# Kernel optimization log

Hardware: AMD Instinct MI355X
Metric: run time of the kernel (lower is better)

Reference implementation:

```python
import jax, jax.numpy as jnp
import numpy as np

NEG_SLOPE = 0.2

def gat_conv(x, src, dst, W, att_src, att_dst, bias, heads, out_c, concat):
    # x: [N, F_in]; src/dst: [E] (self-loops already included)
    N = x.shape[0]
    xh = (x @ W).reshape(N, heads, out_c)               # [N,H,C]
    a_src = jnp.sum(xh * att_src, axis=-1)              # [N,H]
    a_dst = jnp.sum(xh * att_dst, axis=-1)              # [N,H]
    alpha = a_src[src] + a_dst[dst]                     # [E,H]
    alpha = jax.nn.leaky_relu(alpha, NEG_SLOPE)
    # segment softmax over destination node
    m = jax.ops.segment_max(alpha, dst, num_segments=N) # [N,H]
    e = jnp.exp(alpha - m[dst])                         # [E,H]
    s = jax.ops.segment_sum(e, dst, num_segments=N)     # [N,H]
    coef = e / s[dst]                                   # [E,H]
    msg = xh[src] * coef[:, :, None]                    # [E,H,C]
    out = jax.ops.segment_sum(msg, dst, num_segments=N) # [N,H,C]
    if concat:
        out = out.reshape(N, heads * out_c)
    else:
        out = out.mean(axis=1)
    return out + bias

def setup_inputs() -> dict:
    key = jax.random.key(0)
    ks = jax.random.split(key, 12)
    N, E = 50000, 400000
    Fin, Hc, H, Fout = 128, 16, 8, 128
    x = jax.random.normal(ks[0], (N, Fin), dtype=jnp.float32)
    src = jax.random.randint(ks[1], (E,), 0, N, dtype=jnp.int32)
    dst = jax.random.randint(ks[2], (E,), 0, N, dtype=jnp.int32)
    g = lambda k, shp, fan: (jax.random.normal(k, shp, dtype=jnp.float32) * (1.0 / np.sqrt(fan))).astype(jnp.float32)
    return {
        'x': x, 'src': src, 'dst': dst,
        'W1': g(ks[3], (Fin, H * Hc), Fin),
        'att_src1': g(ks[4], (H, Hc), Hc),
        'att_dst1': g(ks[5], (H, Hc), Hc),
        'b1': jnp.zeros((H * Hc,), dtype=jnp.float32),
        'W2': g(ks[6], (H * Hc, Fout), H * Hc),
        'att_src2': g(ks[7], (1, Fout), Fout),
        'att_dst2': g(ks[8], (1, Fout), Fout),
        'b2': jnp.zeros((Fout,), dtype=jnp.float32),
    }

def reference(x, src, dst, W1, att_src1, att_dst1, b1, W2, att_src2, att_dst2, b2):
    N = x.shape[0]
    loops = jnp.arange(N, dtype=src.dtype)
    s = jnp.concatenate([src, loops])  # add_self_loops=True (PyG default)
    d = jnp.concatenate([dst, loops])
    h = gat_conv(x, s, d, W1, att_src1, att_dst1, b1, heads=8, out_c=16, concat=True)
    h = jax.nn.elu(h)
    out = gat_conv(h, s, d, W2, att_src2, att_dst2, b2, heads=1, out_c=128, concat=False)
    return out
```

## Files before the change

kernel.cpp:

```cpp
#include <hip/hip_runtime.h>
#include <hip/hip_bf16.h>
#include <math.h>

#define NEG_SLOPE 0.2f
#define SCAN_BLOCK 256
#define BK 32
#define LOG2E 1.4426950408889634f

__device__ __forceinline__ unsigned pack_bf16_pair(float lo, float hi) {
    unsigned ul = __float_as_uint(lo);
    ul += 0x7fffu + ((ul >> 16) & 1u);
    unsigned uh = __float_as_uint(hi);
    uh += 0x7fffu + ((uh >> 16) & 1u);
    return (ul >> 16) | (uh & 0xffff0000u);
}

__global__ __launch_bounds__(256) void zero_int_kernel(int* __restrict__ p, int n) {
    int i = blockIdx.x * 256 + threadIdx.x;
    if (i < n) p[i] = 0;
}

__global__ __launch_bounds__(256) void count_deg_kernel(const int* __restrict__ dst,
                                                        int E, int N, int* __restrict__ deg) {
    int e = blockIdx.x * 256 + threadIdx.x;
    int Etot = E + N;
    if (e >= Etot) return;
    int d = (e < E) ? dst[e] : (e - E);
    atomicAdd(&deg[d], 1);
}

__global__ __launch_bounds__(SCAN_BLOCK) void deg_partial_kernel(const int* __restrict__ deg,
                                                                 int* __restrict__ part, int N) {
    __shared__ int red[SCAN_BLOCK];
    int t = threadIdx.x;
    int i = blockIdx.x * SCAN_BLOCK + t;
    red[t] = (i < N) ? deg[i] : 0;
    __syncthreads();
    #pragma unroll
    for (int off = SCAN_BLOCK / 2; off > 0; off >>= 1) {
        if (t < off) red[t] += red[t + off];
        __syncthreads();
    }
    if (t == 0) part[blockIdx.x] = red[0];
}

__global__ __launch_bounds__(1024) void scan_part_kernel(int* __restrict__ part, int nPart) {
    __shared__ int s[1024];
    int t = threadIdx.x;
    int v = (t < nPart) ? part[t] : 0;
    s[t] = v;
    __syncthreads();
    for (int off = 1; off < 1024; off <<= 1) {
        int u = (t >= off) ? s[t - off] : 0;
        __syncthreads();
        s[t] += u;
        __syncthreads();
    }
    if (t < nPart) part[t] = (t == 0) ? 0 : s[t - 1];
}

__global__ __launch_bounds__(SCAN_BLOCK) void scan_final_kernel(const int* __restrict__ deg,
                                                                const int* __restrict__ part,
                                                                int* __restrict__ row_ptr, int N) {
    __shared__ int s[SCAN_BLOCK];
    int t = threadIdx.x;
    int i = blockIdx.x * SCAN_BLOCK + t;
    int v = (i < N) ? deg[i] : 0;
    s[t] = v;
    __syncthreads();
    #pragma unroll
    for (int off = 1; off < SCAN_BLOCK; off <<= 1) {
        int u = (t >= off) ? s[t - off] : 0;
        __syncthreads();
        s[t] += u;
        __syncthreads();
    }
    int incl = s[t];
    int base = part[blockIdx.x];
    if (i < N) row_ptr[i] = base + incl - v;
    if (i == N - 1) row_ptr[N] = base + incl;
}

__global__ __launch_bounds__(256) void scatter_kernel(const int* __restrict__ src,
                                                      const int* __restrict__ dst,
                                                      int E, int N,
                                                      const int* __restrict__ row_ptr,
                                                      int* __restrict__ cursor,
                                                      int* __restrict__ col_src) {
    int e = blockIdx.x * 256 + threadIdx.x;
    int Etot = E + N;
    if (e >= Etot) return;
    int d, s;
    if (e < E) { d = dst[e]; s = src[e]; } else { d = e - E; s = e - E; }
    int pos = atomicAdd(&cursor[d], 1);
    col_src[row_ptr[d] + pos] = s;
}

__global__ __launch_bounds__(128) void gemm_rb_kernel(const float* __restrict__ X,
                                                      const float* __restrict__ W,
                                                      float* __restrict__ Y,
                                                      unsigned* __restrict__ Ybf, int N) {
    __shared__ float Xs[BK][68];
    __shared__ float Wt[BK][128];
    const int t = threadIdx.x;
    const int r0 = blockIdx.x * 64;
    const int lane = t & 63, w = t >> 6;
    const int lx = lane & 15, ly = lane >> 4;
    const int row_base = w * 32 + ly * 8;
    const int c1 = lx * 4, c2 = 64 + lx * 4;

    float acc[8][8];
    #pragma unroll
    for (int i = 0; i < 8; ++i)
        #pragma unroll
        for (int j = 0; j < 8; ++j) acc[i][j] = 0.f;

    for (int kt = 0; kt < 128; kt += BK) {
        __syncthreads();
        #pragma unroll
        for (int i = 0; i < 4; ++i) {
            int idx = i * 128 + t;
            int row = idx >> 3, k4 = idx & 7;
            int gr = r0 + row;
            float4 g = make_float4(0.f, 0.f, 0.f, 0.f);
            if (gr < N) g = *(const float4*)(X + (size_t)gr * 128 + kt + k4 * 4);
            Xs[k4 * 4 + 0][row] = g.x;
            Xs[k4 * 4 + 1][row] = g.y;
            Xs[k4 * 4 + 2][row] = g.z;
            Xs[k4 * 4 + 3][row] = g.w;
        }
        #pragma unroll
        for (int i = 0; i < 8; ++i) {
            int idx = i * 128 + t;
            int wr = idx >> 5, c4 = idx & 31;
            *(float4*)&Wt[wr][c4 * 4] = *(const float4*)(W + (size_t)(kt + wr) * 128 + c4 * 4);
        }
        __syncthreads();

        #pragma unroll 8
        for (int k = 0; k < BK; ++k) {
            float4 a0 = *(const float4*)&Xs[k][row_base];
            float4 a1 = *(const float4*)&Xs[k][row_base + 4];
            float4 b0 = *(const float4*)&Wt[k][c1];
            float4 b1 = *(const float4*)&Wt[k][c2];
            float a[8] = {a0.x, a0.y, a0.z, a0.w, a1.x, a1.y, a1.z, a1.w};
            float b[8] = {b0.x, b0.y, b0.z, b0.w, b1.x, b1.y, b1.z, b1.w};
            #pragma unroll
            for (int i = 0; i < 8; ++i)
                #pragma unroll
                for (int j = 0; j < 8; ++j)
                    acc[i][j] = fmaf(a[i], b[j], acc[i][j]);
        }
    }

    #pragma unroll
    for (int i = 0; i < 8; ++i) {
        int gr = r0 + row_base + i;
        if (gr < N) {
            *(float4*)(Y + (size_t)gr * 128 + c1) =
                make_float4(acc[i][0], acc[i][1], acc[i][2], acc[i][3]);
            *(float4*)(Y + (size_t)gr * 128 + c2) =
                make_float4(acc[i][4], acc[i][5], acc[i][6], acc[i][7]);
            uint4 pk;
            pk.x = pack_bf16_pair(acc[i][0], acc[i][4]);
            pk.y = pack_bf16_pair(acc[i][1], acc[i][5]);
            pk.z = pack_bf16_pair(acc[i][2], acc[i][6]);
            pk.w = pack_bf16_pair(acc[i][3], acc[i][7]);
            *(uint4*)(Ybf + (size_t)gr * 64 + c1) = pk;
        }
    }
}

__global__ __launch_bounds__(256) void attdot1_kernel(const float* __restrict__ xh,
                                                      const float* __restrict__ attS,
                                                      const float* __restrict__ attD,
                                                      float* __restrict__ asrc,
                                                      float* __restrict__ adst, int N) {
    int node = blockIdx.x * 4 + (threadIdx.x >> 6);
    int lane = threadIdx.x & 63;
    if (node >= N) return;
    const float* row = xh + (size_t)node * 128;
    float x1 = row[lane], x2 = row[lane + 64];
    float s1 = x1 * attS[lane], s2 = x2 * attS[lane + 64];
    float d1 = x1 * attD[lane], d2 = x2 * attD[lane + 64];
    #pragma unroll
    for (int off = 8; off >= 1; off >>= 1) {
        s1 += __shfl_xor(s1, off, 64);
        s2 += __shfl_xor(s2, off, 64);
        d1 += __shfl_xor(d1, off, 64);
        d2 += __shfl_xor(d2, off, 64);
    }
    if ((lane & 15) == 0) {
        int h = lane >> 4;
        asrc[node * 8 + h]     = s1;
        asrc[node * 8 + h + 4] = s2;
        adst[node * 8 + h]     = d1;
        adst[node * 8 + h + 4] = d2;
    }
}

__global__ __launch_bounds__(256) void attdot2_kernel(const float* __restrict__ xh,
                                                      const float* __restrict__ attS,
                                                      const float* __restrict__ attD,
                                                      float* __restrict__ asrc,
                                                      float* __restrict__ adst, int N) {
    int node = blockIdx.x * 4 + (threadIdx.x >> 6);
    int lane = threadIdx.x & 63;
    if (node >= N) return;
    const float* row = xh + (size_t)node * 128;
    float x1 = row[lane], x2 = row[lane + 64];
    float ts = x1 * attS[lane] + x2 * attS[lane + 64];
    float td = x1 * attD[lane] + x2 * attD[lane + 64];
    #pragma unroll
    for (int off = 32; off >= 1; off >>= 1) {
        ts += __shfl_xor(ts, off, 64);
        td += __shfl_xor(td, off, 64);
    }
    if (lane == 0) { asrc[node] = ts; adst[node] = td; }
}

__global__ __launch_bounds__(256) void agg1_kernel(const unsigned* __restrict__ xhp,
                                                   const float* __restrict__ asrc,
                                                   const float* __restrict__ adst,
                                                   const int* __restrict__ row_ptr,
                                                   const int* __restrict__ col_src,
                                                   const float* __restrict__ b1,
                                                   float* __restrict__ out, int N) {
    int node = blockIdx.x * 4 + (threadIdx.x >> 6);
    int lane = threadIdx.x & 63;
    if (node >= N) return;
    const int grp = lane >> 4;
    const int lx = lane & 15;
    const int gbase = lane & 48;
    float ad1 = adst[node * 8 + grp];
    float ad2 = adst[node * 8 + grp + 4];
    int beg = row_ptr[node], end = row_ptr[node + 1];
    int deg = end - beg;

    float s1 = 0.f, s2 = 0.f, acc1 = 0.f, acc2 = 0.f;

    if (deg <= 16) {
        bool valid = lx < deg;
        int sv = col_src[valid ? (beg + lx) : beg];
        float al1 = asrc[sv * 8 + grp] + ad1;
        float al2 = asrc[sv * 8 + grp + 4] + ad2;
        al1 = fmaxf(al1, NEG_SLOPE * al1);
        al2 = fmaxf(al2, NEG_SLOPE * al2);
        float m1 = valid ? al1 : -1e30f;
        float m2 = valid ? al2 : -1e30f;
        #pragma unroll
        for (int off = 1; off < 16; off <<= 1) {
            m1 = fmaxf(m1, __shfl_xor(m1, off, 64));
            m2 = fmaxf(m2, __shfl_xor(m2, off, 64));
        }
        float p1 = valid ? exp2f((al1 - m1) * LOG2E) : 0.f;
        float p2 = valid ? exp2f((al2 - m2) * LOG2E) : 0.f;
        #pragma unroll 4
        for (int i = 0; i < deg; ++i) {
            int   svi = __shfl(sv, gbase + i, 64);
            float q1  = __shfl(p1, gbase + i, 64);
            float q2  = __shfl(p2, gbase + i, 64);
            unsigned v = xhp[(size_t)svi * 64 + lane];
            float x1 = __uint_as_float(v << 16);
            float x2 = __uint_as_float(v & 0xffff0000u);
            s1 += q1; acc1 = fmaf(q1, x1, acc1);
            s2 += q2; acc2 = fmaf(q2, x2, acc2);
        }
    } else {
        float m1 = -1e30f, m2 = -1e30f;
        for (int c = beg; c < end; c += 16) {
            int e = c + lx;
            bool valid = e < end;
            int sv = col_src[valid ? e : beg];
            float al1 = asrc[sv * 8 + grp] + ad1;
            float al2 = asrc[sv * 8 + grp + 4] + ad2;
            al1 = fmaxf(al1, NEG_SLOPE * al1);
            al2 = fmaxf(al2, NEG_SLOPE * al2);
            if (valid) { m1 = fmaxf(m1, al1); m2 = fmaxf(m2, al2); }
        }
        #pragma unroll
        for (int off = 1; off < 16; off <<= 1) {
            m1 = fmaxf(m1, __shfl_xor(m1, off, 64));
            m2 = fmaxf(m2, __shfl_xor(m2, off, 64));
        }
        for (int c = beg; c < end; c += 16) {
            int e = c + lx;
            bool valid = e < end;
            int sv = col_src[valid ? e : beg];
            float al1 = asrc[sv * 8 + grp] + ad1;
            float al2 = asrc[sv * 8 + grp + 4] + ad2;
            al1 = fmaxf(al1, NEG_SLOPE * al1);
            al2 = fmaxf(al2, NEG_SLOPE * al2);
            float p1 = valid ? exp2f((al1 - m1) * LOG2E) : 0.f;
            float p2 = valid ? exp2f((al2 - m2) * LOG2E) : 0.f;
            int cnt = min(16, end - c);
            #pragma unroll 4
            for (int i = 0; i < cnt; ++i) {
                int   svi = __shfl(sv, gbase + i, 64);
                float q1  = __shfl(p1, gbase + i, 64);
                float q2  = __shfl(p2, gbase + i, 64);
                unsigned v = xhp[(size_t)svi * 64 + lane];
                float x1 = __uint_as_float(v << 16);
                float x2 = __uint_as_float(v & 0xffff0000u);
                s1 += q1; acc1 = fmaf(q1, x1, acc1);
                s2 += q2; acc2 = fmaf(q2, x2, acc2);
            }
        }
    }

    float o1 = acc1 / s1 + b1[lane];
    float o2 = acc2 / s2 + b1[lane + 64];
    o1 = (o1 > 0.f) ? o1 : (__expf(o1) - 1.f);
    o2 = (o2 > 0.f) ? o2 : (__expf(o2) - 1.f);
    out[(size_t)node * 128 + lane]      = o1;
    out[(size_t)node * 128 + lane + 64] = o2;
}

__global__ __launch_bounds__(256) void agg2_kernel(const unsigned* __restrict__ xhp,
                                                   const float* __restrict__ asrc,
                                                   const float* __restrict__ adst,
                                                   const int* __restrict__ row_ptr,
                                                   const int* __restrict__ col_src,
                                                   const float* __restrict__ b2,
                                                   float* __restrict__ out, int N) {
    int node = blockIdx.x * 4 + (threadIdx.x >> 6);
    int lane = threadIdx.x & 63;
    if (node >= N) return;
    float ad = adst[node];
    int beg = row_ptr[node], end = row_ptr[node + 1];
    int deg = end - beg;

    float s = 0.f, acc1 = 0.f, acc2 = 0.f;

    if (deg <= 64) {
        bool valid = lane < deg;
        int sv = col_src[valid ? (beg + lane) : beg];
        float al = asrc[sv] + ad;
        al = fmaxf(al, NEG_SLOPE * al);
        float m = valid ? al : -1e30f;
        #pragma unroll
        for (int off = 1; off < 64; off <<= 1)
            m = fmaxf(m, __shfl_xor(m, off, 64));
        float p = valid ? exp2f((al - m) * LOG2E) : 0.f;
        #pragma unroll 4
        for (int i = 0; i < deg; ++i) {
            int   svi = __shfl(sv, i, 64);
            float q   = __shfl(p, i, 64);
            unsigned v = xhp[(size_t)svi * 64 + lane];
            float x1 = __uint_as_float(v << 16);
            float x2 = __uint_as_float(v & 0xffff0000u);
            s += q;
            acc1 = fmaf(q, x1, acc1);
            acc2 = fmaf(q, x2, acc2);
        }
    } else {
        float m = -1e30f;
        for (int c = beg; c < end; c += 64) {
            int e = c + lane;
            bool valid = e < end;
            int sv = col_src[valid ? e : beg];
            float al = asrc[sv] + ad;
            al = fmaxf(al, NEG_SLOPE * al);
            if (valid) m = fmaxf(m, al);
        }
        #pragma unroll
        for (int off = 1; off < 64; off <<= 1)
            m = fmaxf(m, __shfl_xor(m, off, 64));
        for (int c = beg; c < end; c += 64) {
            int e = c + lane;
            bool valid = e < end;
            int sv = col_src[valid ? e : beg];
            float al = asrc[sv] + ad;
            al = fmaxf(al, NEG_SLOPE * al);
            float p = valid ? exp2f((al - m) * LOG2E) : 0.f;
            int cnt = min(64, end - c);
            #pragma unroll 4
            for (int i = 0; i < cnt; ++i) {
                int   svi = __shfl(sv, i, 64);
                float q   = __shfl(p, i, 64);
                unsigned v = xhp[(size_t)svi * 64 + lane];
                float x1 = __uint_as_float(v << 16);
                float x2 = __uint_as_float(v & 0xffff0000u);
                s += q;
                acc1 = fmaf(q, x1, acc1);
                acc2 = fmaf(q, x2, acc2);
            }
        }
    }

    out[(size_t)node * 128 + lane]      = acc1 / s + b2[lane];
    out[(size_t)node * 128 + lane + 64] = acc2 / s + b2[lane + 64];
}

extern "C" void kernel_launch(void* const* d_in, const int* in_sizes, int n_in,
                              void* d_out, int out_size, void* d_ws, size_t ws_size,
                              hipStream_t stream) {
    const float* x        = (const float*)d_in[0];
    const int*   src      = (const int*)d_in[1];
    const int*   dst      = (const int*)d_in[2];
    const float* W1       = (const float*)d_in[3];
    const float* att_src1 = (const float*)d_in[4];
    const float* att_dst1 = (const float*)d_in[5];
    const float* b1       = (const float*)d_in[6];
    const float* W2       = (const float*)d_in[7];
    const float* att_src2 = (const float*)d_in[8];
    const float* att_dst2 = (const float*)d_in[9];
    const float* b2       = (const float*)d_in[10];

    const int N = in_sizes[0] / 128;
    const int E = in_sizes[1];
    const int Etot = E + N;

    float* fws   = (float*)d_ws;
    float* xh    = fws;
    float* asrc1 = xh + (size_t)N * 128;
    float* adst1 = asrc1 + (size_t)N * 8;
    float* asrc2 = adst1 + (size_t)N * 8;
    float* adst2 = asrc2 + N;
    int*   deg     = (int*)(adst2 + N);
    int*   cursor  = deg + N;
    int*   row_ptr = cursor + N;
    int*   col_src = row_ptr + N + 1;
    int*   part    = col_src + Etot;
    unsigned* xhp  = (unsigned*)(part + 1024);

    float* h = (float*)d_out;

    const int nodeBlocks = (N + 3) / 4;
    const int edgeBlocks = (Etot + 255) / 256;
    const int gemmBlocks = (N + 63) / 64;
    const int scanBlocks = (N + SCAN_BLOCK - 1) / SCAN_BLOCK;

    zero_int_kernel<<<(2 * N + 255) / 256, 256, 0, stream>>>(deg, 2 * N);
    count_deg_kernel<<<edgeBlocks, 256, 0, stream>>>(dst, E, N, deg);
    deg_partial_kernel<<<scanBlocks, SCAN_BLOCK, 0, stream>>>(deg, part, N);
    scan_part_kernel<<<1, 1024, 0, stream>>>(part, scanBlocks);
    scan_final_kernel<<<scanBlocks, SCAN_BLOCK, 0, stream>>>(deg, part, row_ptr, N);
    scatter_kernel<<<edgeBlocks, 256, 0, stream>>>(src, dst, E, N, row_ptr, cursor, col_src);

    gemm_rb_kernel<<<gemmBlocks, 128, 0, stream>>>(x, W1, xh, xhp, N);
    attdot1_kernel<<<nodeBlocks, 256, 0, stream>>>(xh, att_src1, att_dst1, asrc1, adst1, N);
    agg1_kernel<<<nodeBlocks, 256, 0, stream>>>(xhp, asrc1, adst1, row_ptr, col_src, b1, h, N);

    gemm_rb_kernel<<<gemmBlocks, 128, 0, stream>>>(h, W2, xh, xhp, N);
    attdot2_kernel<<<nodeBlocks, 256, 0, stream>>>(xh, att_src2, att_dst2, asrc2, adst2, N);
    agg2_kernel<<<nodeBlocks, 256, 0, stream>>>(xhp, asrc2, adst2, row_ptr, col_src, b2, (float*)d_out, N);
}
```

Baseline: 311.9 us.

## Fuse attention dot products into GEMM epilogue and drop fp32 xh output

The attention-coefficient dot products (a_src, a_dst) are now computed in the GEMM epilogue from register accumulators using shuffles, replacing the separate attdot kernels. The fp32 xh output is no longer written, so only the bf16 copy used by aggregation is stored. The GEMM block also goes to 256 threads with 4x8 tiles per thread to raise occupancy. This removes two launches and a full N x 128 fp32 write and re-read per layer, at the cost of shuffle work in the epilogue and a smaller per-thread tile.

```diff
diff --git a/kernel.cpp b/kernel.cpp
--- a/kernel.cpp
+++ b/kernel.cpp
@@ -96,30 +96,37 @@
     col_src[row_ptr[d] + pos] = s;
 }
 
-__global__ __launch_bounds__(128) void gemm_rb_kernel(const float* __restrict__ X,
-                                                      const float* __restrict__ W,
-                                                      float* __restrict__ Y,
-                                                      unsigned* __restrict__ Ybf, int N) {
+__global__ __launch_bounds__(256) void gemm_fused_kernel(const float* __restrict__ X,
+                                                         const float* __restrict__ W,
+                                                         const float* __restrict__ attS,
+                                                         const float* __restrict__ attD,
+                                                         unsigned* __restrict__ Ybf,
+                                                         float* __restrict__ asrc,
+                                                         float* __restrict__ adst,
+                                                         int N, int heads) {
     __shared__ float Xs[BK][68];
     __shared__ float Wt[BK][128];
+    __shared__ float attSs[128], attDs[128];
     const int t = threadIdx.x;
     const int r0 = blockIdx.x * 64;
-    const int lane = t & 63, w = t >> 6;
+    const int lane = t & 63, wv = t >> 6;
     const int lx = lane & 15, ly = lane >> 4;
-    const int row_base = w * 32 + ly * 8;
+    const int row_base = wv * 16 + ly * 4;
     const int c1 = lx * 4, c2 = 64 + lx * 4;
 
-    float acc[8][8];
+    if (t < 128) { attSs[t] = attS[t]; attDs[t] = attD[t]; }
+
+    float acc[4][8];
     #pragma unroll
-    for (int i = 0; i < 8; ++i)
+    for (int i = 0; i < 4; ++i)
         #pragma unroll
         for (int j = 0; j < 8; ++j) acc[i][j] = 0.f;
 
     for (int kt = 0; kt < 128; kt += BK) {
         __syncthreads();
         #pragma unroll
-        for (int i = 0; i < 4; ++i) {
-            int idx = i * 128 + t;
+        for (int i = 0; i < 2; ++i) {
+            int idx = i * 256 + t;
             int row = idx >> 3, k4 = idx & 7;
             int gr = r0 + row;
             float4 g = make_float4(0.f, 0.f, 0.f, 0.f);
@@ -130,8 +137,8 @@
             Xs[k4 * 4 + 3][row] = g.w;
         }
         #pragma unroll
-        for (int i = 0; i < 8; ++i) {
-            int idx = i * 128 + t;
+        for (int i = 0; i < 4; ++i) {
+            int idx = i * 256 + t;
             int wr = idx >> 5, c4 = idx & 31;
             *(float4*)&Wt[wr][c4 * 4] = *(const float4*)(W + (size_t)(kt + wr) * 128 + c4 * 4);
         }
@@ -140,13 +147,12 @@
         #pragma unroll 8
         for (int k = 0; k < BK; ++k) {
             float4 a0 = *(const float4*)&Xs[k][row_base];
-            float4 a1 = *(const float4*)&Xs[k][row_base + 4];
             float4 b0 = *(const float4*)&Wt[k][c1];
             float4 b1 = *(const float4*)&Wt[k][c2];
-            float a[8] = {a0.x, a0.y, a0.z, a0.w, a1.x, a1.y, a1.z, a1.w};
+            float a[4] = {a0.x, a0.y, a0.z, a0.w};
             float b[8] = {b0.x, b0.y, b0.z, b0.w, b1.x, b1.y, b1.z, b1.w};
             #pragma unroll
-            for (int i = 0; i < 8; ++i)
+            for (int i = 0; i < 4; ++i)
                 #pragma unroll
                 for (int j = 0; j < 8; ++j)
                     acc[i][j] = fmaf(a[i], b[j], acc[i][j]);
@@ -154,13 +160,10 @@
     }
 
     #pragma unroll
-    for (int i = 0; i < 8; ++i) {
+    for (int i = 0; i < 4; ++i) {
         int gr = r0 + row_base + i;
-        if (gr < N) {
-            *(float4*)(Y + (size_t)gr * 128 + c1) =
-                make_float4(acc[i][0], acc[i][1], acc[i][2], acc[i][3]);
-            *(float4*)(Y + (size_t)gr * 128 + c2) =
-                make_float4(acc[i][4], acc[i][5], acc[i][6], acc[i][7]);
+        bool ok = gr < N;
+        if (ok) {
             uint4 pk;
             pk.x = pack_bf16_pair(acc[i][0], acc[i][4]);
             pk.y = pack_bf16_pair(acc[i][1], acc[i][5]);
@@ -168,55 +171,43 @@
             pk.w = pack_bf16_pair(acc[i][3], acc[i][7]);
             *(uint4*)(Ybf + (size_t)gr * 64 + c1) = pk;
         }
-    }
-}
-
-__global__ __launch_bounds__(256) void attdot1_kernel(const float* __restrict__ xh,
-                                                      const float* __restrict__ attS,
-                                                      const float* __restrict__ attD,
-                                                      float* __restrict__ asrc,
-                                                      float* __restrict__ adst, int N) {
-    int node = blockIdx.x * 4 + (threadIdx.x >> 6);
-    int lane = threadIdx.x & 63;
-    if (node >= N) return;
-    const float* row = xh + (size_t)node * 128;
-    float x1 = row[lane], x2 = row[lane + 64];
-    float s1 = x1 * attS[lane], s2 = x2 * attS[lane + 64];
-    float d1 = x1 * attD[lane], d2 = x2 * attD[lane + 64];
-    #pragma unroll
-    for (int off = 8; off >= 1; off >>= 1) {
-        s1 += __shfl_xor(s1, off, 64);
-        s2 += __shfl_xor(s2, off, 64);
-        d1 += __shfl_xor(d1, off, 64);
-        d2 += __shfl_xor(d2, off, 64);
-    }
-    if ((lane & 15) == 0) {
-        int h = lane >> 4;
-        asrc[node * 8 + h]     = s1;
-        asrc[node * 8 + h + 4] = s2;
-        adst[node * 8 + h]     = d1;
-        adst[node * 8 + h + 4] = d2;
-    }
-}
-
-__global__ __launch_bounds__(256) void attdot2_kernel(const float* __restrict__ xh,
-                                                      const float* __restrict__ attS,
-                                                      const float* __restrict__ attD,
-                                                      float* __restrict__ asrc,
-                                                      float* __restrict__ adst, int N) {
-    int node = blockIdx.x * 4 + (threadIdx.x >> 6);
-    int lane = threadIdx.x & 63;
-    if (node >= N) return;
-    const float* row = xh + (size_t)node * 128;
-    float x1 = row[lane], x2 = row[lane + 64];
-    float ts = x1 * attS[lane] + x2 * attS[lane + 64];
-    float td = x1 * attD[lane] + x2 * attD[lane + 64];
-    #pragma unroll
-    for (int off = 32; off >= 1; off >>= 1) {
-        ts += __shfl_xor(ts, off, 64);
-        td += __shfl_xor(td, off, 64);
-    }
-    if (lane == 0) { asrc[node] = ts; adst[node] = td; }
+        if (heads == 8) {
+            float s0 = 0.f, s1 = 0.f, d0 = 0.f, d1 = 0.f;
+            #pragma unroll
+            for (int j = 0; j < 4; ++j) {
+                s0 = fmaf(acc[i][j],     attSs[c1 + j], s0);
+                d0 = fmaf(acc[i][j],     attDs[c1 + j], d0);
+                s1 = fmaf(acc[i][4 + j], attSs[c2 + j], s1);
+                d1 = fmaf(acc[i][4 + j], attDs[c2 + j], d1);
+            }
+            s0 += __shfl_xor(s0, 1, 64); s0 += __shfl_xor(s0, 2, 64);
+            s1 += __shfl_xor(s1, 1, 64); s1 += __shfl_xor(s1, 2, 64);
+            d0 += __shfl_xor(d0, 1, 64); d0 += __shfl_xor(d0, 2, 64);
+            d1 += __shfl_xor(d1, 1, 64); d1 += __shfl_xor(d1, 2, 64);
+            if (ok && (lx & 3) == 0) {
+                int hA = lx >> 2;
+                asrc[gr * 8 + hA]     = s0;
+                asrc[gr * 8 + hA + 4] = s1;
+                adst[gr * 8 + hA]     = d0;
+                adst[gr * 8 + hA + 4] = d1;
+            }
+        } else {
+            float sp = 0.f, dp = 0.f;
+            #pragma unroll
+            for (int j = 0; j < 4; ++j) {
+                sp = fmaf(acc[i][j],     attSs[c1 + j], sp);
+                sp = fmaf(acc[i][4 + j], attSs[c2 + j], sp);
+                dp = fmaf(acc[i][j],     attDs[c1 + j], dp);
+                dp = fmaf(acc[i][4 + j], attDs[c2 + j], dp);
+            }
+            #pragma unroll
+            for (int off = 1; off < 16; off <<= 1) {
+                sp += __shfl_xor(sp, off, 64);
+                dp += __shfl_xor(dp, off, 64);
+            }
+            if (ok && lx == 0) { asrc[gr] = sp; adst[gr] = dp; }
+        }
+    }
 }
 
 __global__ __launch_bounds__(256) void agg1_kernel(const unsigned* __restrict__ xhp,
@@ -412,8 +403,7 @@
     const int Etot = E + N;
 
     float* fws   = (float*)d_ws;
-    float* xh    = fws;
-    float* asrc1 = xh + (size_t)N * 128;
+    float* asrc1 = fws;
     float* adst1 = asrc1 + (size_t)N * 8;
     float* asrc2 = adst1 + (size_t)N * 8;
     float* adst2 = asrc2 + N;
@@ -438,11 +428,9 @@
     scan_final_kernel<<<scanBlocks, SCAN_BLOCK, 0, stream>>>(deg, part, row_ptr, N);
     scatter_kernel<<<edgeBlocks, 256, 0, stream>>>(src, dst, E, N, row_ptr, cursor, col_src);
 
-    gemm_rb_kernel<<<gemmBlocks, 128, 0, stream>>>(x, W1, xh, xhp, N);
-    attdot1_kernel<<<nodeBlocks, 256, 0, stream>>>(xh, att_src1, att_dst1, asrc1, adst1, N);
+    gemm_fused_kernel<<<gemmBlocks, 256, 0, stream>>>(x, W1, att_src1, att_dst1, xhp, asrc1, adst1, N, 8);
     agg1_kernel<<<nodeBlocks, 256, 0, stream>>>(xhp, asrc1, adst1, row_ptr, col_src, b1, h, N);
 
-    gemm_rb_kernel<<<gemmBlocks, 128, 0, stream>>>(h, W2, xh, xhp, N);
-    attdot2_kernel<<<nodeBlocks, 256, 0, stream>>>(xh, att_src2, att_dst2, asrc2, adst2, N);
+    gemm_fused_kernel<<<gemmBlocks, 256, 0, stream>>>(h, W2, att_src2, att_dst2, xhp, asrc2, adst2, N, 1);
     agg2_kernel<<<nodeBlocks, 256, 0, stream>>>(xhp, asrc2, adst2, row_ptr, col_src, b2, (float*)d_out, N);
 }
```

Result: faster. 282.1 us (-9.5%).
